# Performance work log

Hardware: AMD Instinct MI355X
Metric: run time of the kernel (lower is better)

Reference implementation:

```python
import jax, jax.numpy as jnp
import numpy as np

B, S = 8192, 4096
EPS = 1e-6
ALPHA, BETA = 0.1, 0.1


def setup_inputs() -> dict:
    key = jax.random.key(0)
    k1, k2, k3, k4 = jax.random.split(key, 4)
    yhat = jax.random.normal(k1, (B, S), dtype=jnp.float32)
    y_dense = jax.random.normal(k2, (B, S), dtype=jnp.float32)
    keep = jax.random.bernoulli(k3, 0.5, (B, S))
    y = jnp.where(keep, y_dense, 0.0)
    # neighbor matrix: entries remapped {1.0->alpha, 2.0->beta}, mostly zero
    r = jax.random.randint(k4, (S, S), 0, 10)
    W = jnp.where(r == 1, ALPHA, jnp.where(r == 2, BETA, 0.0)).astype(jnp.float32)
    return {"yhat": yhat, "y": y, "W": W}


def reference(yhat, y, W):
    mask = (y != 0).astype(yhat.dtype)            # [B, S] nonzero-target mask
    sq = jnp.square(y - yhat)                      # [B, S] squared error
    # per-column loop `df_spatial_loss[:, i] = squared_error @ W[i]` == sq @ W.T
    spatial = sq @ W.T                             # [B, S] spatial regularization
    total = (sq + spatial) * mask                  # gather-at-nonzero == masking
    # mean over the nonzero entries only, then sqrt (RMSE)
    loss = jnp.sqrt(total.sum() / mask.sum() + EPS)
    return loss
```

## Files before the change

### kernel.cpp

```cpp
#include <hip/hip_runtime.h>
#include <math.h>

typedef unsigned long long u64;
typedef unsigned int u32;
typedef unsigned char u8;
typedef __attribute__((ext_vector_type(2))) unsigned long long u64x2;
typedef __attribute__((ext_vector_type(4))) int i32x4;

#define NB 8192
#define NS 4096

static const size_t OFF_CNT = 0;
static const size_t OFF_P3  = 16384;
static const size_t OFF_M8  = 32768;
static const size_t OFF_BT  = OFF_M8 + (size_t)NB * NS;
static const size_t WS_NEED = OFF_BT + (size_t)NS * NS;
static const size_t OFF_MB  = 32768;
static const size_t OFF_WB  = OFF_MB + (size_t)64 * NB * 8;

__device__ __forceinline__ void gload_lds16(const void* g, void* l) {
    __builtin_amdgcn_global_load_lds(
        (const __attribute__((address_space(1))) unsigned int*)g,
        (__attribute__((address_space(3))) unsigned int*)l, 16, 0, 0);
}


__global__ __launch_bounds__(256) void k12_prep(
    const float* __restrict__ y, const float* __restrict__ W,
    u32* __restrict__ m8, u32* __restrict__ bt, u64* __restrict__ pcnt)
{
    const int g = blockIdx.x;
    const int t = threadIdx.x;
    if (g < 2048) {
        __shared__ unsigned rc[4];
        const float4* y4 = (const float4*)y;
        size_t base = (size_t)g * 4096 + t;
        unsigned lcnt = 0;
        #pragma unroll 4
        for (int k = 0; k < 16; ++k) {
            float4 v = y4[base + (size_t)k * 256];
            unsigned b0 = v.x != 0.0f, b1 = v.y != 0.0f, b2 = v.z != 0.0f, b3 = v.w != 0.0f;
            lcnt += b0 + b1 + b2 + b3;
            m8[base + (size_t)k * 256] = b0 | (b1 << 8) | (b2 << 16) | (b3 << 24);
        }
        for (int off = 32; off; off >>= 1) lcnt += __shfl_down(lcnt, off, 64);
        if ((t & 63) == 0) rc[t >> 6] = lcnt;
        __syncthreads();
        if (t == 0) pcnt[g] = (u64)rc[0] + rc[1] + rc[2] + rc[3];
    } else {
        __shared__ float tile[64][65];
        const int gg = g - 2048;
        const int j0 = (gg & 63) * 64, i0 = (gg >> 6) * 64;
        #pragma unroll
        for (int k = 0; k < 16; ++k) {
            int lin = t + (k << 8);
            int r = lin >> 6, c = lin & 63;
            tile[r][c] = W[(size_t)(i0 + r) * NS + (j0 + c)];
        }
        __syncthreads();
        const int jj = t >> 2, ck = t & 3;
        u32 wd[4];
        #pragma unroll
        for (int gq = 0; gq < 4; ++gq) {
            u32 u = 0;
            #pragma unroll
            for (int bb = 0; bb < 4; ++bb)
                u |= (tile[ck * 16 + gq * 4 + bb][jj] != 0.0f ? 1u : 0u) << (8 * bb);
            wd[gq] = u;
        }
        uint4 out = make_uint4(wd[0], wd[1], wd[2], wd[3]);
        *(uint4*)&bt[(((size_t)(j0 + jj) << 12) + (size_t)(i0 + ck * 16)) >> 2] = out;
    }
}

__global__ __launch_bounds__(256) void k3b_mfma(
    const float* __restrict__ y, const float* __restrict__ yhat,
    const u8* __restrict__ m8, const u8* __restrict__ bt,
    double* __restrict__ p3)
{
    __shared__ alignas(16) u8 lds[2][16384];
    const int b0 = blockIdx.x << 7;
    const int j0 = blockIdx.y << 7;
    const int t = threadIdx.x, l = t & 63, wv = t >> 6;
    const int wr = wv >> 1, wc = wv & 1;

    const int row4 = t >> 2, pos = t & 3;
    const int chunk = pos ^ ((row4 >> 1) & 3);
    const u8* srcA = m8 + ((size_t)(b0 + row4) << 12) + ((size_t)chunk << 4);
    const u8* srcB = bt + ((size_t)(j0 + row4) << 12) + ((size_t)chunk << 4);

    const int slot = ((l >> 4) ^ ((l >> 1) & 3)) & 3;
    const int frbase = ((wr << 6) + (l & 15)) * 64 + (slot << 4);
    const int fcbase = 8192 + ((wc << 6) + (l & 15)) * 64 + (slot << 4);

    i32x4 acc[4][4];
    #pragma unroll
    for (int i = 0; i < 4; ++i)
        #pragma unroll
        for (int j = 0; j < 4; ++j) acc[i][j] = (i32x4){0, 0, 0, 0};

    auto stage = [&](int s, int buf) {
        const u8* sA = srcA + (s << 6);
        const u8* sB = srcB + (s << 6);
        u8* dA = &lds[buf][(size_t)wv << 10];
        u8* dB = &lds[buf][8192 + ((size_t)wv << 10)];
        gload_lds16(sA, dA);
        gload_lds16(sA + ((size_t)64 << 12), dA + 4096);
        gload_lds16(sB, dB);
        gload_lds16(sB + ((size_t)64 << 12), dB + 4096);
    };

    stage(0, 0);
    __syncthreads();

    #pragma unroll 1
    for (int ks = 0; ks < 64; ++ks) {
        const int cb = ks & 1;
        if (ks < 63) stage(ks + 1, cb ^ 1);
        const u8* L = lds[cb];
        i32x4 a[4], b[4];
        #pragma unroll
        for (int f = 0; f < 4; ++f) {
            a[f] = *(const i32x4*)&L[frbase + f * 1024];
            b[f] = *(const i32x4*)&L[fcbase + f * 1024];
        }
        #pragma unroll
        for (int fr = 0; fr < 4; ++fr)
            #pragma unroll
            for (int fc = 0; fc < 4; ++fc)
                acc[fr][fc] = __builtin_amdgcn_mfma_i32_16x16x64_i8(
                    a[fr], b[fc], acc[fr][fc], 0, 0, 0);
        __syncthreads();
    }

    float part = 0.0f;
    const int col = j0 + (wc << 6) + (l & 15);
    #pragma unroll
    for (int fr = 0; fr < 4; ++fr)
        #pragma unroll
        for (int q = 0; q < 4; ++q) {
            size_t rbase = ((size_t)(b0 + (wr << 6) + (fr << 4) + ((l >> 4) << 2) + q) << 12) + col;
            #pragma unroll
            for (int fc = 0; fc < 4; ++fc) {
                float yv = y[rbase + (fc << 4)];
                float hv = yhat[rbase + (fc << 4)];
                float e = yv - hv;
                float wgt = 0.1f * (float)acc[fr][fc][q] + (yv != 0.0f ? 1.0f : 0.0f);
                part = fmaf(e * e, wgt, part);
            }
        }

    for (int off = 32; off; off >>= 1) part += __shfl_down(part, off, 64);
    float* red = (float*)lds;
    __syncthreads();
    if ((t & 63) == 0) red[t >> 6] = part;
    __syncthreads();
    if (t == 0)
        p3[(size_t)blockIdx.y * gridDim.x + blockIdx.x] =
            (double)red[0] + (double)red[1] + (double)red[2] + (double)red[3];
}


__global__ __launch_bounds__(256) void k1_pack_mask(
    const float* __restrict__ y, u64* __restrict__ mbT, u64* __restrict__ pcnt)
{
    __shared__ unsigned rc[4];
    const unsigned t = threadIdx.x;
    const unsigned lane = t & 63;
    const float4* y4 = (const float4*)y;
    u64 qi = (u64)blockIdx.x * 256 + t;
    const u64 stride = (u64)2048 * 256;
    unsigned lcnt = 0;
    #pragma unroll 4
    for (int it = 0; it < 16; ++it, qi += stride) {
        float4 v = y4[qi];
        u64 b0 = __ballot(v.x != 0.0f);
        u64 b1 = __ballot(v.y != 0.0f);
        u64 b2 = __ballot(v.z != 0.0f);
        u64 b3 = __ballot(v.w != 0.0f);
        lcnt += (v.x != 0.0f) + (v.y != 0.0f) + (v.z != 0.0f) + (v.w != 0.0f);
        if (lane < 4) {
            unsigned sh = lane << 4;
            u64 word = ((b0 >> sh) & 0xFFFFull)
                     | (((b1 >> sh) & 0xFFFFull) << 16)
                     | (((b2 >> sh) & 0xFFFFull) << 32)
                     | (((b3 >> sh) & 0xFFFFull) << 48);
            u64 gw = ((qi - lane) >> 4) + lane;
            mbT[((gw & 63) << 13) + (gw >> 6)] = word;
        }
    }
    for (int off = 32; off; off >>= 1) lcnt += __shfl_down(lcnt, off, 64);
    if ((t & 63) == 0) rc[t >> 6] = lcnt;
    __syncthreads();
    if (t == 0) pcnt[blockIdx.x] = (u64)rc[0] + rc[1] + rc[2] + rc[3];
}

__global__ __launch_bounds__(256) void k2_pack_w(
    const float* __restrict__ W, u64* __restrict__ wbT)
{
    __shared__ float tile[64][65];
    const int j0 = blockIdx.x * 64;
    const int w  = blockIdx.y;
    const int i0 = w * 64;
    const int t = threadIdx.x;
    #pragma unroll
    for (int k = 0; k < 16; ++k) {
        int lin = t + (k << 8);
        int r = lin >> 6, c = lin & 63;
        tile[r][c] = W[(size_t)(i0 + r) * NS + (j0 + c)];
    }
    __syncthreads();
    const int lane = t & 63;
    const int wvv = t >> 6;
    const int pr = ((lane & 15) << 2) + (lane >> 4);
    for (int jj = wvv; jj < 64; jj += 4) {
        u64 bal = __ballot(tile[pr][jj] != 0.0f);
        if (lane == 0) wbT[((size_t)w << 12) + (j0 + jj)] = bal;
    }
}

__global__ __launch_bounds__(256) void k3_main(
    const float* __restrict__ y, const float* __restrict__ yhat,
    const u64* __restrict__ mbT, const u64* __restrict__ wbT,
    double* __restrict__ p3)
{
    __shared__ alignas(16) u64 mT[16 * 128];
    __shared__ alignas(16) u64 wT[16 * 128];
    const int b0 = blockIdx.x << 7;
    const int j0 = blockIdx.y << 7;
    const int t  = threadIdx.x;
    const int r0 = (t >> 4) << 3;
    const int cj = t & 15;
    const unsigned sx = ((unsigned)cj >> 2) << 4;

    unsigned cnt[8][8];
    #pragma unroll
    for (int a = 0; a < 8; ++a)
        #pragma unroll
        for (int b = 0; b < 8; ++b) cnt[a][b] = 0;

    char* mB = (char*)mT;
    char* wB = (char*)wT;

    #pragma unroll 1
    for (int s = 0; s < 4; ++s) {
        u64x2 gm[4], gq[4];
        #pragma unroll
        for (int k = 0; k < 4; ++k) {
            int lin = t + (k << 8);
            int wl = (s << 4) + (lin >> 6), c2 = lin & 63;
            gm[k] = *(const u64x2*)&mbT[((size_t)wl << 13) + b0 + 2 * c2];
            gq[k] = *(const u64x2*)&wbT[((size_t)wl << 12) + j0 + 2 * c2];
        }
        __syncthreads();
        #pragma unroll
        for (int k = 0; k < 4; ++k) {
            int lin = t + (k << 8);
            int wl = lin >> 6, c2 = lin & 63;
            int p = c2 ^ ((c2 >> 4) & 3);
            *(u64x2*)(mB + (wl << 10) + (c2 << 4)) = gm[k];
            *(u64x2*)(wB + (wl << 10) + (p << 4)) = gq[k];
        }
        __syncthreads();

        unsigned mo = (unsigned)(r0 << 3);
        unsigned qs = (unsigned)(cj << 6) + sx;
        #pragma unroll 2
        for (int w = 0; w < 16; ++w) {
            unsigned ml[16], ql[16];
            #pragma unroll
            for (int k = 0; k < 4; ++k) {
                uint4 a = *(const uint4*)(mB + mo + (k << 4));
                ml[4 * k + 0] = a.x; ml[4 * k + 1] = a.y;
                ml[4 * k + 2] = a.z; ml[4 * k + 3] = a.w;
                uint4 b = *(const uint4*)(wB + (qs ^ (unsigned)(k << 4)));
                ql[4 * k + 0] = b.x; ql[4 * k + 1] = b.y;
                ql[4 * k + 2] = b.z; ql[4 * k + 3] = b.w;
            }
            #pragma unroll
            for (int aa = 0; aa < 8; ++aa)
                #pragma unroll
                for (int bb = 0; bb < 8; ++bb) {
                    unsigned x0 = ml[2 * aa] & ql[2 * bb];
                    unsigned x1 = ml[2 * aa + 1] & ql[2 * bb + 1];
                    asm("v_bcnt_u32_b32 %0, %1, %0" : "+v"(cnt[aa][bb]) : "v"(x0));
                    asm("v_bcnt_u32_b32 %0, %1, %0" : "+v"(cnt[aa][bb]) : "v"(x1));
                }
            mo += 1024; qs += 1024;
        }
    }

    float part = 0.0f;
    const int c0 = cj << 3;
    #pragma unroll
    for (int aa = 0; aa < 8; ++aa) {
        size_t off = ((size_t)(b0 + r0 + aa) << 12) + (size_t)(j0 + c0);
        float ys[8], hs[8];
        *(float4*)&ys[0] = *(const float4*)(y + off);
        *(float4*)&ys[4] = *(const float4*)(y + off + 4);
        *(float4*)&hs[0] = *(const float4*)(yhat + off);
        *(float4*)&hs[4] = *(const float4*)(yhat + off + 4);
        #pragma unroll
        for (int bb = 0; bb < 8; ++bb) {
            float e = ys[bb] - hs[bb];
            float wgt = 0.1f * (float)cnt[aa][bb] + (ys[bb] != 0.0f ? 1.0f : 0.0f);
            part = fmaf(e * e, wgt, part);
        }
    }

    for (int off = 32; off; off >>= 1) part += __shfl_down(part, off, 64);
    float* red = (float*)mT;
    __syncthreads();
    if ((t & 63) == 0) red[t >> 6] = part;
    __syncthreads();
    if (t == 0)
        p3[(size_t)blockIdx.y * gridDim.x + blockIdx.x] =
            (double)red[0] + (double)red[1] + (double)red[2] + (double)red[3];
}

__global__ __launch_bounds__(256) void k4_final(
    const u64* __restrict__ pcnt, const double* __restrict__ p3, float* __restrict__ out)
{
    __shared__ double rs[4];
    __shared__ u64 rcc[4];
    double s3 = 0.0;
    u64 c = 0;
    for (int i = threadIdx.x; i < 2048; i += 256) { s3 += p3[i]; c += pcnt[i]; }
    for (int off = 32; off; off >>= 1) {
        s3 += __shfl_down(s3, off, 64);
        c  += __shfl_down(c, off, 64);
    }
    int wv = threadIdx.x >> 6;
    if ((threadIdx.x & 63) == 0) { rs[wv] = s3; rcc[wv] = c; }
    __syncthreads();
    if (threadIdx.x == 0) {
        double S3 = rs[0] + rs[1] + rs[2] + rs[3];
        double C  = (double)(rcc[0] + rcc[1] + rcc[2] + rcc[3]);
        out[0] = (float)sqrt(S3 / C + 1e-6);
    }
}

extern "C" void kernel_launch(void* const* d_in, const int* in_sizes, int n_in,
                              void* d_out, int out_size, void* d_ws, size_t ws_size,
                              hipStream_t stream) {
    const float* yhat = (const float*)d_in[0];
    const float* y    = (const float*)d_in[1];
    const float* W    = (const float*)d_in[2];
    char* ws = (char*)d_ws;
    u64*    pcnt = (u64*)(ws + OFF_CNT);
    double* p3   = (double*)(ws + OFF_P3);

    if (ws_size >= WS_NEED) {
        u32* m8 = (u32*)(ws + OFF_M8);
        u32* bt = (u32*)(ws + OFF_BT);
        k12_prep<<<dim3(2048 + 4096), dim3(256), 0, stream>>>(y, W, m8, bt, pcnt);
        k3b_mfma<<<dim3(64, 32), dim3(256), 0, stream>>>(
            y, yhat, (const u8*)m8, (const u8*)bt, p3);
        k4_final<<<dim3(1), dim3(256), 0, stream>>>(pcnt, p3, (float*)d_out);
    } else {
        u64* mbT = (u64*)(ws + OFF_MB);
        u64* wbT = (u64*)(ws + OFF_WB);
        k1_pack_mask<<<dim3(2048), dim3(256), 0, stream>>>(y, mbT, pcnt);
        k2_pack_w<<<dim3(64, 64), dim3(256), 0, stream>>>(W, wbT);
        k3_main<<<dim3(64, 32), dim3(256), 0, stream>>>(y, yhat, mbT, wbT, p3);
        k4_final<<<dim3(1), dim3(256), 0, stream>>>(pcnt, p3, (float*)d_out);
    }
}
```

Baseline: 222.6 us.

## Enlarge int8 MFMA block tile to 256x256 with deeper prefetch and setprio

The MFMA spatial-count kernel moves from 128x128 tiles with 256 threads to 256x256 tiles with 512 threads. Each K step now covers 128 bytes, uses a new XOR-swizzled LDS layout, and keeps two stages in flight with explicit vmcnt waits and raw barriers. MFMA bursts are wrapped in s_setprio, and the final reduction is adjusted for the smaller grid. The goal is to halve the global/L2 reloads of the packed mask and W operands and to hide load latency better. The cost is 128 KB of LDS per block, which limits occupancy to one block per CU, plus larger accumulator register pressure.

```diff
diff --git a/kernel.cpp b/kernel.cpp
--- a/kernel.cpp
+++ b/kernel.cpp
@@ -73,73 +73,107 @@
     }
 }
 
-__global__ __launch_bounds__(256) void k3b_mfma(
+__global__ __launch_bounds__(512, 2) void k3g_mfma(
     const float* __restrict__ y, const float* __restrict__ yhat,
     const u8* __restrict__ m8, const u8* __restrict__ bt,
     double* __restrict__ p3)
 {
-    __shared__ alignas(16) u8 lds[2][16384];
-    const int b0 = blockIdx.x << 7;
-    const int j0 = blockIdx.y << 7;
+    __shared__ alignas(16) u8 lds[2][65536];
+    const int b0 = blockIdx.x << 8;
+    const int j0 = blockIdx.y << 8;
     const int t = threadIdx.x, l = t & 63, wv = t >> 6;
-    const int wr = wv >> 1, wc = wv & 1;
-
-    const int row4 = t >> 2, pos = t & 3;
-    const int chunk = pos ^ ((row4 >> 1) & 3);
-    const u8* srcA = m8 + ((size_t)(b0 + row4) << 12) + ((size_t)chunk << 4);
-    const u8* srcB = bt + ((size_t)(j0 + row4) << 12) + ((size_t)chunk << 4);
-
-    const int slot = ((l >> 4) ^ ((l >> 1) & 3)) & 3;
-    const int frbase = ((wr << 6) + (l & 15)) * 64 + (slot << 4);
-    const int fcbase = 8192 + ((wc << 6) + (l & 15)) * 64 + (slot << 4);
-
-    i32x4 acc[4][4];
+    const int wr = wv >> 2, wc = wv & 3;
+
+    const int srow = t >> 3;
+    const int schunk = (t & 7) ^ (srow & 7);
+    const u8* sA = m8 + ((size_t)(b0 + srow) << 12) + ((size_t)schunk << 4);
+    const u8* sB = bt + ((size_t)(j0 + srow) << 12) + ((size_t)schunk << 4);
+
+    const int rl = l & 15, qh = l >> 4, rx = l & 7;
+    const int sb0 = (((0 + qh) ^ rx) << 4);
+    const int sb1 = (((4 + qh) ^ rx) << 4);
+
+    i32x4 acc[8][4];
     #pragma unroll
-    for (int i = 0; i < 4; ++i)
+    for (int i = 0; i < 8; ++i)
         #pragma unroll
         for (int j = 0; j < 4; ++j) acc[i][j] = (i32x4){0, 0, 0, 0};
 
-    auto stage = [&](int s, int buf) {
-        const u8* sA = srcA + (s << 6);
-        const u8* sB = srcB + (s << 6);
-        u8* dA = &lds[buf][(size_t)wv << 10];
-        u8* dB = &lds[buf][8192 + ((size_t)wv << 10)];
-        gload_lds16(sA, dA);
-        gload_lds16(sA + ((size_t)64 << 12), dA + 4096);
-        gload_lds16(sB, dB);
-        gload_lds16(sB + ((size_t)64 << 12), dB + 4096);
+    auto stage = [&](int kt2, int buf) {
+        const size_t ko = (size_t)kt2 << 7;
+        u8* dst = &lds[buf][0];
+        #pragma unroll
+        for (int h = 0; h < 2; ++h)
+            #pragma unroll
+            for (int c = 0; c < 2; ++c) {
+                const size_t roff = ((size_t)(h * 128 + c * 64) << 12);
+                u8* d = dst + h * 16384 + c * 8192 + (wv << 10);
+                gload_lds16(sA + roff + ko, d);
+                gload_lds16(sB + roff + ko, d + 32768);
+            }
     };
 
     stage(0, 0);
-    __syncthreads();
+    stage(1, 1);
+    asm volatile("s_waitcnt vmcnt(8)" ::: "memory");
+    __builtin_amdgcn_s_barrier();
+    asm volatile("" ::: "memory");
 
     #pragma unroll 1
-    for (int ks = 0; ks < 64; ++ks) {
-        const int cb = ks & 1;
-        if (ks < 63) stage(ks + 1, cb ^ 1);
-        const u8* L = lds[cb];
-        i32x4 a[4], b[4];
-        #pragma unroll
-        for (int f = 0; f < 4; ++f) {
-            a[f] = *(const i32x4*)&L[frbase + f * 1024];
-            b[f] = *(const i32x4*)&L[fcbase + f * 1024];
-        }
-        #pragma unroll
-        for (int fr = 0; fr < 4; ++fr)
-            #pragma unroll
-            for (int fc = 0; fc < 4; ++fc)
-                acc[fr][fc] = __builtin_amdgcn_mfma_i32_16x16x64_i8(
-                    a[fr], b[fc], acc[fr][fc], 0, 0, 0);
-        __syncthreads();
+    for (int kt = 0; kt < 32; ++kt) {
+        const u8* L = lds[kt & 1];
+
+        i32x4 b[4][2];
+        #pragma unroll
+        for (int fc = 0; fc < 4; ++fc) {
+            const int cbyte = 32768 + (((wc << 6) + (fc << 4) + rl) << 7);
+            b[fc][0] = *(const i32x4*)&L[cbyte + sb0];
+            b[fc][1] = *(const i32x4*)&L[cbyte + sb1];
+        }
+        #pragma unroll
+        for (int q = 0; q < 4; ++q) {
+            i32x4 a[2][2];
+            #pragma unroll
+            for (int i = 0; i < 2; ++i) {
+                const int abyte = (((wr << 7) + ((2 * q + i) << 4) + rl) << 7);
+                a[i][0] = *(const i32x4*)&L[abyte + sb0];
+                a[i][1] = *(const i32x4*)&L[abyte + sb1];
+            }
+            __builtin_amdgcn_s_setprio(1);
+            #pragma unroll
+            for (int i = 0; i < 2; ++i)
+                #pragma unroll
+                for (int fc = 0; fc < 4; ++fc) {
+                    acc[2 * q + i][fc] = __builtin_amdgcn_mfma_i32_16x16x64_i8(
+                        a[i][0], b[fc][0], acc[2 * q + i][fc], 0, 0, 0);
+                    acc[2 * q + i][fc] = __builtin_amdgcn_mfma_i32_16x16x64_i8(
+                        a[i][1], b[fc][1], acc[2 * q + i][fc], 0, 0, 0);
+                }
+            __builtin_amdgcn_s_setprio(0);
+        }
+
+        if (kt < 31) {
+            asm volatile("" ::: "memory");
+            __builtin_amdgcn_s_barrier();
+            asm volatile("" ::: "memory");
+            if (kt < 30) {
+                stage(kt + 2, kt & 1);
+                asm volatile("s_waitcnt vmcnt(8)" ::: "memory");
+            } else {
+                asm volatile("s_waitcnt vmcnt(0)" ::: "memory");
+            }
+            __builtin_amdgcn_s_barrier();
+            asm volatile("" ::: "memory");
+        }
     }
 
     float part = 0.0f;
-    const int col = j0 + (wc << 6) + (l & 15);
+    const int col = j0 + (wc << 6) + rl;
     #pragma unroll
-    for (int fr = 0; fr < 4; ++fr)
+    for (int fr = 0; fr < 8; ++fr)
         #pragma unroll
         for (int q = 0; q < 4; ++q) {
-            size_t rbase = ((size_t)(b0 + (wr << 6) + (fr << 4) + ((l >> 4) << 2) + q) << 12) + col;
+            size_t rbase = ((size_t)(b0 + (wr << 7) + (fr << 4) + (qh << 2) + q) << 12) + col;
             #pragma unroll
             for (int fc = 0; fc < 4; ++fc) {
                 float yv = y[rbase + (fc << 4)];
@@ -155,9 +189,12 @@
     __syncthreads();
     if ((t & 63) == 0) red[t >> 6] = part;
     __syncthreads();
-    if (t == 0)
-        p3[(size_t)blockIdx.y * gridDim.x + blockIdx.x] =
-            (double)red[0] + (double)red[1] + (double)red[2] + (double)red[3];
+    if (t == 0) {
+        float s = 0.0f;
+        #pragma unroll
+        for (int i = 0; i < 8; ++i) s += red[i];
+        p3[(size_t)blockIdx.y * gridDim.x + blockIdx.x] = (double)s;
+    }
 }
 
 
@@ -319,13 +356,15 @@
 }
 
 __global__ __launch_bounds__(256) void k4_final(
-    const u64* __restrict__ pcnt, const double* __restrict__ p3, float* __restrict__ out)
+    const u64* __restrict__ pcnt, const double* __restrict__ p3, float* __restrict__ out,
+    int np3)
 {
     __shared__ double rs[4];
     __shared__ u64 rcc[4];
     double s3 = 0.0;
     u64 c = 0;
-    for (int i = threadIdx.x; i < 2048; i += 256) { s3 += p3[i]; c += pcnt[i]; }
+    for (int i = threadIdx.x; i < 2048; i += 256) c += pcnt[i];
+    for (int i = threadIdx.x; i < np3; i += 256) s3 += p3[i];
     for (int off = 32; off; off >>= 1) {
         s3 += __shfl_down(s3, off, 64);
         c  += __shfl_down(c, off, 64);
@@ -354,15 +393,15 @@
         u32* m8 = (u32*)(ws + OFF_M8);
         u32* bt = (u32*)(ws + OFF_BT);
         k12_prep<<<dim3(2048 + 4096), dim3(256), 0, stream>>>(y, W, m8, bt, pcnt);
-        k3b_mfma<<<dim3(64, 32), dim3(256), 0, stream>>>(
+        k3g_mfma<<<dim3(32, 16), dim3(512), 0, stream>>>(
             y, yhat, (const u8*)m8, (const u8*)bt, p3);
-        k4_final<<<dim3(1), dim3(256), 0, stream>>>(pcnt, p3, (float*)d_out);
+        k4_final<<<dim3(1), dim3(256), 0, stream>>>(pcnt, p3, (float*)d_out, 512);
     } else {
         u64* mbT = (u64*)(ws + OFF_MB);
         u64* wbT = (u64*)(ws + OFF_WB);
         k1_pack_mask<<<dim3(2048), dim3(256), 0, stream>>>(y, mbT, pcnt);
         k2_pack_w<<<dim3(64, 64), dim3(256), 0, stream>>>(W, wbT);
         k3_main<<<dim3(64, 32), dim3(256), 0, stream>>>(y, yhat, mbT, wbT, p3);
-        k4_final<<<dim3(1), dim3(256), 0, stream>>>(pcnt, p3, (float*)d_out);
-    }
-}
+        k4_final<<<dim3(1), dim3(256), 0, stream>>>(pcnt, p3, (float*)d_out, 2048);
+    }
+}
```

Result: faster. 200.2 us (-10.1%).
